# Optimization experiments

Hardware: AMD Instinct MI355X
Metric: run time of the kernel (lower is better)

## Reference

```python
import jax, jax.numpy as jnp
import numpy as np

N_NODES = 50000
N_EDGES = 800000
D_FEAT = 64
UNITS = 64


def setup_inputs() -> dict:
    key = jax.random.key(0)
    k1, k2, k3, k4, k5 = jax.random.split(key, 5)
    embeddings = jax.random.normal(k1, (N_NODES, D_FEAT), dtype=jnp.float32)
    edge_src = jax.random.randint(k2, (N_EDGES,), 0, N_NODES, dtype=jnp.int32)
    edge_dst = jax.random.randint(k3, (N_EDGES,), 0, N_NODES, dtype=jnp.int32)
    # normalized-adjacency-like positive weights
    edge_w = jax.random.uniform(k4, (N_EDGES,), dtype=jnp.float32)
    # keras 'truncated_normal' initializer default stddev=0.05 (approx w/ normal)
    kernel = jax.random.normal(k5, (D_FEAT, UNITS), dtype=jnp.float32) * 0.05
    return {"embeddings": embeddings, "edge_src": edge_src,
            "edge_dst": edge_dst, "edge_w": edge_w, "kernel": kernel}


def reference(embeddings, edge_src, edge_dst, edge_w, kernel):
    # SpMM: agg[i] = sum_{e: dst(e)=i} w_e * embeddings[src(e)]
    msgs = embeddings[edge_src] * edge_w[:, None]            # [E, D]
    agg = jax.ops.segment_sum(msgs, edge_dst,
                              num_segments=embeddings.shape[0])  # [N, D]
    # dense GEMM + relu (use_bias=False)
    return jax.nn.relu(agg @ kernel)                          # [N, units]
```

## Files before the change

### kernel.cpp

```cpp
#include <hip/hip_runtime.h>
#include <hip/hip_bf16.h>

#define D     64
#define CH    4096
#define BKT   32
#define PASS  1024
#define CAP   1024
#define CAPSH 10

__global__ __launch_bounds__(256) void front(
    const float* __restrict__ emb,
    const float* __restrict__ W,
    __hip_bfloat16* __restrict__ Zb,
    const int*   __restrict__ src,
    const int*   __restrict__ dst,
    const float* __restrict__ w,
    int*         __restrict__ gcnt,
    int2*        __restrict__ csr,
    int N, int E, int NB, int NC)
{
    __shared__ int2 rec[CH];
    __shared__ int  lcnt[1568];
    __shared__ int  sh[256];

    const int t = threadIdx.x;

    if ((int)blockIdx.x < NC) {
        const int c   = blockIdx.x;
        const int e0  = c * CH;
        const int cnt = min(CH, E - e0);

        for (int b = t; b < NB; b += 256) lcnt[b] = 0;
        __syncthreads();

        int2 myrec[16]; int mypos[16];
        const int4*   s4p = reinterpret_cast<const int4*>(src + e0);
        const int4*   d4p = reinterpret_cast<const int4*>(dst + e0);
        const float4* w4p = reinterpret_cast<const float4*>(w + e0);
#pragma unroll
        for (int i = 0; i < 4; ++i) {
            int g = i * 256 + t;
            if (g * 4 < cnt) {
                int4   s4 = s4p[g];
                int4   d4 = d4p[g];
                float4 w4 = w4p[g];
                int b0 = d4.x >> 5, b1 = d4.y >> 5, b2 = d4.z >> 5, b3 = d4.w >> 5;
                myrec[4*i+0] = make_int2(s4.x | ((d4.x & 31) << 16) | (b0 << 21), __float_as_int(w4.x));
                myrec[4*i+1] = make_int2(s4.y | ((d4.y & 31) << 16) | (b1 << 21), __float_as_int(w4.y));
                myrec[4*i+2] = make_int2(s4.z | ((d4.z & 31) << 16) | (b2 << 21), __float_as_int(w4.z));
                myrec[4*i+3] = make_int2(s4.w | ((d4.w & 31) << 16) | (b3 << 21), __float_as_int(w4.w));
                mypos[4*i+0] = atomicAdd(&lcnt[b0], 1);
                mypos[4*i+1] = atomicAdd(&lcnt[b1], 1);
                mypos[4*i+2] = atomicAdd(&lcnt[b2], 1);
                mypos[4*i+3] = atomicAdd(&lcnt[b3], 1);
            } else {
#pragma unroll
                for (int k = 0; k < 4; ++k) mypos[4*i+k] = -1;
            }
        }
        __syncthreads();

        int hv[7], ps[7], gbase[7];
        const int hbase = t * 7;
#pragma unroll
        for (int k = 0; k < 7; ++k) {
            int b = hbase + k;
            hv[k] = (b < NB) ? lcnt[b] : 0;
        }
#pragma unroll
        for (int k = 0; k < 7; ++k)
            gbase[k] = (hv[k] > 0) ? atomicAdd(&gcnt[hbase + k], hv[k]) : 0;

        int s = 0;
#pragma unroll
        for (int k = 0; k < 7; ++k) { ps[k] = s; s += hv[k]; }
        sh[t] = s;
        __syncthreads();
        for (int off = 1; off < 256; off <<= 1) {
            int x = (t >= off) ? sh[t - off] : 0;
            __syncthreads();
            sh[t] += x;
            __syncthreads();
        }
        const int hexcl = sh[t] - s;
        __syncthreads();
#pragma unroll
        for (int k = 0; k < 7; ++k) {
            int b = hbase + k;
            if (b < NB) lcnt[b] = hexcl + ps[k];
        }
        __syncthreads();

#pragma unroll
        for (int k = 0; k < 16; ++k) {
            if (mypos[k] >= 0)
                rec[lcnt[(unsigned)myrec[k].x >> 21] + mypos[k]] = myrec[k];
        }
        __syncthreads();

#pragma unroll
        for (int k = 0; k < 7; ++k) {
            int b = hbase + k;
            if (b < NB) lcnt[b] = (b << CAPSH) + gbase[k] - (hexcl + ps[k]);
        }
        __syncthreads();

        for (int j = t; j < cnt; j += 256) {
            int2 rj = rec[j];
            csr[j + lcnt[(unsigned)rj.x >> 21]] = rj;
        }
        return;
    }

    float* At = (float*)rec;
    const int row0 = ((int)blockIdx.x - NC) * 64;
    const int lane = t & 63;
    const int wave = t >> 6;

    float wcol[D];
#pragma unroll
    for (int k = 0; k < D; ++k) wcol[k] = W[k * D + lane];

    for (int i = t; i < 1024; i += 256) {
        int r = i >> 4, gr = row0 + r;
        float4 v = (gr < N)
            ? reinterpret_cast<const float4*>(emb)[(size_t)gr * 16 + (i & 15)]
            : float4{0.f, 0.f, 0.f, 0.f};
        reinterpret_cast<float4*>(At)[i] = v;
    }
    __syncthreads();

    for (int rr = 0; rr < 16; ++rr) {
        int r = wave * 16 + rr, gr = row0 + r;
        if (gr >= N) break;
        const float4* arow = reinterpret_cast<const float4*>(At + r * D);
        float acc = 0.f;
#pragma unroll
        for (int k4 = 0; k4 < 16; ++k4) {
            float4 a = arow[k4];
            acc = fmaf(a.x, wcol[4 * k4 + 0], acc);
            acc = fmaf(a.y, wcol[4 * k4 + 1], acc);
            acc = fmaf(a.z, wcol[4 * k4 + 2], acc);
            acc = fmaf(a.w, wcol[4 * k4 + 3], acc);
        }
        Zb[(size_t)gr * D + lane] = __float2bfloat16(acc);
    }
}

__global__ __launch_bounds__(256) void aggregate(
    const __hip_bfloat16* __restrict__ Zb,
    const int2* __restrict__ csr,
    const int*  __restrict__ gcnt,
    float*      __restrict__ out,
    int N, int NB)
{
    __shared__ int2 srec[PASS];
    __shared__ int  hist[BKT];
    __shared__ int  nbase[BKT + 1];

    const int t = threadIdx.x;
    const int b = blockIdx.x;

    const int bStart = b << CAPSH;
    const int bEnd   = bStart + gcnt[b];

    const int wv = t >> 6, lane = t & 63, slot = lane >> 3, q = lane & 7;
    const int4* Zq = reinterpret_cast<const int4*>(Zb);

    float4 alo[8], ahi[8];
#pragma unroll
    for (int r = 0; r < 8; ++r) { alo[r] = float4{0,0,0,0}; ahi[r] = float4{0,0,0,0}; }

#define FMA8(LO, HI, WW, ZZ)                                                     \
    do {                                                                         \
        (LO).x = fmaf((WW), __uint_as_float((unsigned)(ZZ).x << 16),        (LO).x); \
        (LO).y = fmaf((WW), __uint_as_float((unsigned)(ZZ).x & 0xFFFF0000u),(LO).y); \
        (LO).z = fmaf((WW), __uint_as_float((unsigned)(ZZ).y << 16),        (LO).z); \
        (LO).w = fmaf((WW), __uint_as_float((unsigned)(ZZ).y & 0xFFFF0000u),(LO).w); \
        (HI).x = fmaf((WW), __uint_as_float((unsigned)(ZZ).z << 16),        (HI).x); \
        (HI).y = fmaf((WW), __uint_as_float((unsigned)(ZZ).z & 0xFFFF0000u),(HI).y); \
        (HI).z = fmaf((WW), __uint_as_float((unsigned)(ZZ).w << 16),        (HI).z); \
        (HI).w = fmaf((WW), __uint_as_float((unsigned)(ZZ).w & 0xFFFF0000u),(HI).w); \
    } while (0)

    for (int cur = bStart; cur < bEnd; cur += PASS) {
        const int cnt = min(PASS, bEnd - cur);
        if (t < BKT) hist[t] = 0;
        __syncthreads();

        int2 myrec[4]; int mypos[4];
#pragma unroll
        for (int k = 0; k < 4; ++k) {
            int j = k * 256 + t;
            if (j < cnt) {
                int2 r2 = csr[cur + j];
                myrec[k] = r2;
                mypos[k] = atomicAdd(&hist[(r2.x >> 16) & (BKT - 1)], 1);
            } else mypos[k] = -1;
        }
        __syncthreads();

        if (t < BKT) {
            int v = hist[t], x = v;
            for (int off = 1; off < BKT; off <<= 1) {
                int y = __shfl_up(x, off, 64);
                if (t >= off) x += y;
            }
            nbase[t] = x - v;
            if (t == BKT - 1) nbase[BKT] = x;
        }
        __syncthreads();

#pragma unroll
        for (int k = 0; k < 4; ++k) {
            if (mypos[k] >= 0)
                srec[nbase[(myrec[k].x >> 16) & (BKT - 1)] + mypos[k]] = myrec[k];
        }
        __syncthreads();

        for (int r = 0; r < 8; ++r) {
            const int nl = wv * 8 + r;
            const int jb = nbase[nl] + slot;
            const int je = nbase[nl + 1];
            const int j1 = jb + 8, j2 = jb + 16;
            int2 e0 = make_int2(0, 0), e1 = make_int2(0, 0), e2 = make_int2(0, 0);
            if (jb < je) e0 = srec[jb];
            if (j1 < je) e1 = srec[j1];
            if (j2 < je) e2 = srec[j2];
            int4 z0 = make_int4(0,0,0,0), z1 = make_int4(0,0,0,0), z2 = make_int4(0,0,0,0);
            if (jb < je) z0 = Zq[(size_t)(e0.x & 0xFFFF) * 8 + q];
            if (j1 < je) z1 = Zq[(size_t)(e1.x & 0xFFFF) * 8 + q];
            if (j2 < je) z2 = Zq[(size_t)(e2.x & 0xFFFF) * 8 + q];
            FMA8(alo[r], ahi[r], __int_as_float(e0.y), z0);
            FMA8(alo[r], ahi[r], __int_as_float(e1.y), z1);
            FMA8(alo[r], ahi[r], __int_as_float(e2.y), z2);
            for (int j = j2 + 8; j < je; j += 8) {
                int2 e = srec[j];
                int4 zz = Zq[(size_t)(e.x & 0xFFFF) * 8 + q];
                FMA8(alo[r], ahi[r], __int_as_float(e.y), zz);
            }
        }
        __syncthreads();
    }

    const int node0 = b * BKT + wv * 8;
#pragma unroll
    for (int r = 0; r < 8; ++r) {
        float4 lo = alo[r], hi = ahi[r];
#pragma unroll
        for (int off = 32; off >= 8; off >>= 1) {
            lo.x += __shfl_down(lo.x, off, 64);
            lo.y += __shfl_down(lo.y, off, 64);
            lo.z += __shfl_down(lo.z, off, 64);
            lo.w += __shfl_down(lo.w, off, 64);
            hi.x += __shfl_down(hi.x, off, 64);
            hi.y += __shfl_down(hi.y, off, 64);
            hi.z += __shfl_down(hi.z, off, 64);
            hi.w += __shfl_down(hi.w, off, 64);
        }
        int node = node0 + r;
        if (lane < 8 && node < N) {
            float4 o0, o1;
            o0.x = fmaxf(lo.x, 0.f); o0.y = fmaxf(lo.y, 0.f);
            o0.z = fmaxf(lo.z, 0.f); o0.w = fmaxf(lo.w, 0.f);
            o1.x = fmaxf(hi.x, 0.f); o1.y = fmaxf(hi.y, 0.f);
            o1.z = fmaxf(hi.z, 0.f); o1.w = fmaxf(hi.w, 0.f);
            float4* orow = reinterpret_cast<float4*>(out) + (size_t)node * 16 + lane * 2;
            orow[0] = o0;
            orow[1] = o1;
        }
    }
#undef FMA8
}

extern "C" void kernel_launch(void* const* d_in, const int* in_sizes, int n_in,
                              void* d_out, int out_size, void* d_ws, size_t ws_size,
                              hipStream_t stream)
{
    const float* emb  = (const float*)d_in[0];
    const int*   esrc = (const int*)  d_in[1];
    const int*   edst = (const int*)  d_in[2];
    const float* ew   = (const float*)d_in[3];
    const float* W    = (const float*)d_in[4];
    float*       out  = (float*)d_out;

    const int N = in_sizes[0] / D;
    const int E = in_sizes[1];

    const int NB        = (N + BKT - 1) / BKT;
    const int NC        = (E + CH - 1) / CH;
    const int gemmTiles = (N + 63) / 64;

    char* p = (char*)d_ws;
    __hip_bfloat16* Zb = (__hip_bfloat16*)p;  p += (size_t)N * D * 2;
    int*  gcnt = (int*)p;                     p += (size_t)((NB + 3) & ~3) * 4;
    int2* csr  = (int2*)p;

    hipMemsetAsync(gcnt, 0, (size_t)NB * sizeof(int), stream);

    front<<<NC + gemmTiles, 256, 0, stream>>>(
        emb, W, Zb, esrc, edst, ew, gcnt, csr, N, E, NB, NC);

    aggregate<<<NB, 256, 0, stream>>>(
        Zb, csr, gcnt, out, N, NB);
}
```

Before: 144.5 us.

## Split bucket counters into 16 colors to reduce global atomic contention

Each edge chunk block now picks a color from its block index and does its atomicAdd on a per-color copy of the bucket counter. The CSR buffer is split into per-color sub-slots of capacity 128. The goal is to spread contention on the same global counter across 196 chunk blocks and to make the scattered writes more local. In exchange, the aggregate kernel must prefix-sum 16 counts per bucket and map each virtual index to its color segment with a 15-compare search, which adds index arithmetic and non-contiguous reads. The smaller per-slot capacity also makes overflow more likely under skewed degree distributions.

```diff
diff --git a/kernel.cpp b/kernel.cpp
--- a/kernel.cpp
+++ b/kernel.cpp
@@ -1,12 +1,14 @@
 #include <hip/hip_runtime.h>
 #include <hip/hip_bf16.h>
 
-#define D     64
-#define CH    4096
-#define BKT   32
-#define PASS  1024
-#define CAP   1024
-#define CAPSH 10
+#define D       64
+#define CH      4096
+#define BKT     32
+#define PASS    1024
+#define NCOL    16
+#define COLMASK 15
+#define SCAP    128
+#define SCAPSH  7
 
 __global__ __launch_bounds__(256) void front(
     const float* __restrict__ emb,
@@ -26,9 +28,10 @@
     const int t = threadIdx.x;
 
     if ((int)blockIdx.x < NC) {
-        const int c   = blockIdx.x;
-        const int e0  = c * CH;
-        const int cnt = min(CH, E - e0);
+        const int c     = blockIdx.x;
+        const int color = c & COLMASK;
+        const int e0    = c * CH;
+        const int cnt   = min(CH, E - e0);
 
         for (int b = t; b < NB; b += 256) lcnt[b] = 0;
         __syncthreads();
@@ -69,7 +72,8 @@
         }
 #pragma unroll
         for (int k = 0; k < 7; ++k)
-            gbase[k] = (hv[k] > 0) ? atomicAdd(&gcnt[hbase + k], hv[k]) : 0;
+            gbase[k] = (hv[k] > 0)
+                ? atomicAdd(&gcnt[color * NB + hbase + k], hv[k]) : 0;
 
         int s = 0;
 #pragma unroll
@@ -101,7 +105,8 @@
 #pragma unroll
         for (int k = 0; k < 7; ++k) {
             int b = hbase + k;
-            if (b < NB) lcnt[b] = (b << CAPSH) + gbase[k] - (hexcl + ps[k]);
+            if (b < NB)
+                lcnt[b] = ((color * NB + b) << SCAPSH) + gbase[k] - (hexcl + ps[k]);
         }
         __syncthreads();
 
@@ -157,12 +162,19 @@
     __shared__ int2 srec[PASS];
     __shared__ int  hist[BKT];
     __shared__ int  nbase[BKT + 1];
+    __shared__ int  cpre[NCOL + 1];
 
     const int t = threadIdx.x;
     const int b = blockIdx.x;
 
-    const int bStart = b << CAPSH;
-    const int bEnd   = bStart + gcnt[b];
+    if (t == 0) {
+        int s = 0;
+#pragma unroll
+        for (int k = 0; k < NCOL; ++k) { cpre[k] = s; s += gcnt[k * NB + b]; }
+        cpre[NCOL] = s;
+    }
+    __syncthreads();
+    const int T = cpre[NCOL];
 
     const int wv = t >> 6, lane = t & 63, slot = lane >> 3, q = lane & 7;
     const int4* Zq = reinterpret_cast<const int4*>(Zb);
@@ -183,8 +195,8 @@
         (HI).w = fmaf((WW), __uint_as_float((unsigned)(ZZ).w & 0xFFFF0000u),(HI).w); \
     } while (0)
 
-    for (int cur = bStart; cur < bEnd; cur += PASS) {
-        const int cnt = min(PASS, bEnd - cur);
+    for (int cur = 0; cur < T; cur += PASS) {
+        const int cnt = min(PASS, T - cur);
         if (t < BKT) hist[t] = 0;
         __syncthreads();
 
@@ -193,7 +205,11 @@
         for (int k = 0; k < 4; ++k) {
             int j = k * 256 + t;
             if (j < cnt) {
-                int2 r2 = csr[cur + j];
+                int vj = cur + j;
+                int kk = 0;
+#pragma unroll
+                for (int m = 1; m < NCOL; ++m) kk += (vj >= cpre[m]);
+                int2 r2 = csr[((kk * NB + b) << SCAPSH) + (vj - cpre[kk])];
                 myrec[k] = r2;
                 mypos[k] = atomicAdd(&hist[(r2.x >> 16) & (BKT - 1)], 1);
             } else mypos[k] = -1;
@@ -293,10 +309,10 @@
 
     char* p = (char*)d_ws;
     __hip_bfloat16* Zb = (__hip_bfloat16*)p;  p += (size_t)N * D * 2;
-    int*  gcnt = (int*)p;                     p += (size_t)((NB + 3) & ~3) * 4;
+    int*  gcnt = (int*)p;                     p += (size_t)NCOL * ((NB + 3) & ~3) * 4;
     int2* csr  = (int2*)p;
 
-    hipMemsetAsync(gcnt, 0, (size_t)NB * sizeof(int), stream);
+    hipMemsetAsync(gcnt, 0, (size_t)NCOL * NB * sizeof(int), stream);
 
     front<<<NC + gemmTiles, 256, 0, stream>>>(
         emb, W, Zb, esrc, edst, ew, gcnt, csr, N, E, NB, NC);
```

After: 127.6 us. 11.7% less time.
